# Performance work log

Measured on AMD Instinct MI355X. Metric: run time of the kernel, lower is better.

## Reference

```python
import jax, jax.numpy as jnp
import numpy as np
import math

D_MODEL = 512

def setup_inputs() -> dict:
    key = jax.random.key(0)
    k1, k2, k3 = jax.random.split(key, 3)
    X = jax.random.normal(k1, (4, 8192, D_MODEL), dtype=jnp.float32)
    # nn.Linear(d, d, bias=False) weights, applied as x @ W.T
    s = 1.0 / math.sqrt(D_MODEL)
    W_v = jax.random.uniform(k2, (D_MODEL, D_MODEL), dtype=jnp.float32, minval=-s, maxval=s)
    W_theta = jax.random.uniform(k3, (D_MODEL, D_MODEL), dtype=jnp.float32, minval=-s, maxval=s)
    return {"X": X, "W_v": W_v, "W_theta": W_theta}

def reference(X, W_v, W_theta):
    # X: [B, n, d]
    n = X.shape[1]
    d = X.shape[2]
    XW_v = X @ W_v.T            # [B, n, d]
    theta_X = X @ W_theta.T     # [B, n, d]
    # first term: (1/n) * ones(n,n) @ XW_v == column mean broadcast over rows
    first_term = jnp.mean(XW_v, axis=1, keepdims=True)  # [B, 1, d], broadcasts
    # second term: (1/(n*sqrt(d))) * (X @ theta_X^T) @ XW_v
    # associativity-reduced: theta_X^T @ XW_v is [B, d, d]
    kv = jnp.einsum('bnd,bne->bde', theta_X, XW_v)       # [B, d, d]
    second_term = (X @ kv) / (n * math.sqrt(d))          # [B, n, d]
    return first_term + second_term
```

## Files before the change

kernel.cpp:

```cpp
#include <hip/hip_runtime.h>
#include <stdint.h>


typedef __bf16 bf16x8 __attribute__((ext_vector_type(8)));
typedef float f32x4 __attribute__((ext_vector_type(4)));
typedef unsigned short u16x4 __attribute__((ext_vector_type(4)));
typedef unsigned short u16x8 __attribute__((ext_vector_type(8)));

#define BM 128
#define BN 128
#define BK 32

__device__ __forceinline__ unsigned short f2bf(float f) {
  union { float f; unsigned int u; } c; c.f = f;
  unsigned int u = c.u;
  return (unsigned short)((u + 0x7FFFu + ((u >> 16) & 1u)) >> 16);
}
__device__ __forceinline__ float bf2f(unsigned short h) {
  union { unsigned int u; float f; } c; c.u = ((unsigned int)h) << 16;
  return c.f;
}

__device__ __forceinline__ void gld16(const void* g, void* l) {
  using gptr_t = const __attribute__((address_space(1))) void*;
  using lptr_t = __attribute__((address_space(3))) void*;
  __builtin_amdgcn_global_load_lds((gptr_t)(uintptr_t)g,
                                   (lptr_t)(uint32_t)(uintptr_t)l, 16, 0, 0);
}

__device__ __forceinline__ void gemm_tile(const unsigned short* __restrict__ A, int lda,
                                          const unsigned short* __restrict__ B, int ldb,
                                          int K, int m0, int n0, f32x4 (&acc)[4][4],
                                          bool sameAB) {
  __shared__ unsigned short sA[2][BM * BK];
  __shared__ unsigned short sB[2][BN * BK];
  const int tid = threadIdx.x;
  const int lane = tid & 63;
  const int w = tid >> 6;
  const int wm = w >> 1, wn = w & 1;
  const int quad = lane >> 4, l16 = lane & 15;

#pragma unroll
  for (int mi = 0; mi < 4; mi++)
#pragma unroll
    for (int ni = 0; ni < 4; ni++) acc[mi][ni] = f32x4{0.f, 0.f, 0.f, 0.f};

  for (int kt = 0; kt < K; kt += 2 * BK) {
#pragma unroll
    for (int h = 0; h < 2; h++) {
#pragma unroll
      for (int j = 0; j < 2; j++) {
        const int slot = w * 128 + j * 64 + lane;
        const int row = slot >> 2;
        const int col = (slot & 3) * 8;
        const int kc = kt + h * BK + col;
        gld16(A + (size_t)(m0 + row) * lda + kc,
              (char*)sA[h] + (size_t)(w * 128 + j * 64) * 16);
        if (!sameAB)
          gld16(B + (size_t)(n0 + row) * ldb + kc,
                (char*)sB[h] + (size_t)(w * 128 + j * 64) * 16);
      }
    }
    __syncthreads();

#pragma unroll
    for (int h = 0; h < 2; h++) {
      const unsigned short* bs = sameAB ? sA[h] : sB[h];
      bf16x8 af[4], bfr[4];
#pragma unroll
      for (int mi = 0; mi < 4; mi++)
        af[mi] = *(const bf16x8*)&sA[h][(wm * 64 + mi * 16 + l16) * BK + quad * 8];
#pragma unroll
      for (int ni = 0; ni < 4; ni++)
        bfr[ni] = *(const bf16x8*)&bs[(wn * 64 + ni * 16 + l16) * BK + quad * 8];
#pragma unroll
      for (int mi = 0; mi < 4; mi++)
#pragma unroll
        for (int ni = 0; ni < 4; ni++)
          acc[mi][ni] = __builtin_amdgcn_mfma_f32_16x16x32_bf16(af[mi], bfr[ni],
                                                                acc[mi][ni], 0, 0, 0);
    }
    __syncthreads();
  }
}

__global__ __launch_bounds__(256) void prep_kernel(const float* __restrict__ X,
                                                   unsigned short* __restrict__ Xb,
                                                   unsigned short* __restrict__ Xt) {
  __shared__ unsigned short sT[64 * 64];
  const int t = threadIdx.x;
  const int n0 = blockIdx.x * 64, d0 = blockIdx.y * 64;
  const int b = n0 >> 13, nb = n0 & 8191;
  const int r0 = (t >> 4) * 4, c0 = (t & 15) * 4;
  f32x4 v[4];
#pragma unroll
  for (int i = 0; i < 4; i++)
    v[i] = *(const f32x4*)(X + (size_t)(n0 + r0 + i) * 512 + d0 + c0);
#pragma unroll
  for (int i = 0; i < 4; i++) {
    u16x4 o;
#pragma unroll
    for (int j = 0; j < 4; j++) o[j] = f2bf(v[i][j]);
    *(u16x4*)(Xb + (size_t)(n0 + r0 + i) * 512 + d0 + c0) = o;
  }
#pragma unroll
  for (int j = 0; j < 4; j++) {
    u16x4 wv;
#pragma unroll
    for (int i = 0; i < 4; i++) wv[i] = f2bf(v[i][j]);
    const int c = c0 + j;
    const int rsw = r0 ^ (c & 0x38);
    *(u16x4*)&sT[c * 64 + rsw] = wv;
  }
  __syncthreads();
  const int cr = t >> 3, p = t & 7;
#pragma unroll
  for (int h = 0; h < 2; h++) {
    const int c = cr + h * 32;
    const int phys = (p * 8) ^ (c & 0x38);
    u16x8 val = *(const u16x8*)&sT[c * 64 + phys];
    *(u16x8*)(Xt + (size_t)(b * 512 + d0 + c) * 8192 + nb + p * 8) = val;
  }
}

__global__ __launch_bounds__(256) void prep_w_kernel(const float* __restrict__ Wv,
                                                     const float* __restrict__ Wth,
                                                     unsigned short* __restrict__ Wvb,
                                                     unsigned short* __restrict__ Wtb) {
  const int blk = blockIdx.x;
  const int t = threadIdx.x;
  const float* src = (blk < 128) ? Wv : Wth;
  unsigned short* dst = (blk < 128) ? Wvb : Wtb;
  const int i = (blk & 127) * 256 + t;
  const f32x4* pp = (const f32x4*)(src + (size_t)i * 8);
  f32x4 v0 = pp[0], v1 = pp[1];
  u16x8 o;
  o[0] = f2bf(v0[0]); o[1] = f2bf(v0[1]); o[2] = f2bf(v0[2]); o[3] = f2bf(v0[3]);
  o[4] = f2bf(v1[0]); o[5] = f2bf(v1[1]); o[6] = f2bf(v1[2]); o[7] = f2bf(v1[3]);
  *(u16x8*)(dst + (size_t)i * 8) = o;
}

static __device__ const int TI[10] = {0, 0, 0, 0, 1, 1, 1, 2, 2, 3};
static __device__ const int TJ[10] = {0, 1, 2, 3, 1, 2, 3, 2, 3, 3};

__global__ __launch_bounds__(256) void g_gemm_kernel(const unsigned short* __restrict__ Xt,
                                                     float* __restrict__ G_part) {
  const int t = blockIdx.x;
  const int z = blockIdx.y;
  const int b = z >> 4, s = z & 15;
  const int m0 = TI[t] * 128, n0 = TJ[t] * 128;
  const unsigned short* A = Xt + (size_t)b * 512 * 8192 + (size_t)s * 512;
  f32x4 acc[4][4];
  gemm_tile(A, 8192, A, 8192, 512, m0, n0, acc, m0 == n0);
  float* Cp = G_part + ((size_t)z * 10 + t) * 16384;
  const int tid = threadIdx.x, lane = tid & 63, w = tid >> 6;
  const int wm = w >> 1, wn = w & 1, quad = lane >> 4, l16 = lane & 15;
#pragma unroll
  for (int mi = 0; mi < 4; mi++)
#pragma unroll
    for (int ni = 0; ni < 4; ni++) {
      const int ml = wm * 64 + mi * 16 + quad * 4;
      const int nl = wn * 64 + ni * 16 + l16;
      *(f32x4*)(Cp + (size_t)nl * 128 + ml) = acc[mi][ni];
    }
}

__global__ __launch_bounds__(256) void g_fin_kernel(const float* __restrict__ G_part,
                                                    unsigned short* __restrict__ Gb) {
  const int blk = blockIdx.x;
  const int b = blk / 80, rem = blk % 80;
  const int t = rem >> 3, cc = rem & 7;
  const int i = TI[t], j = TJ[t];
  const int m0 = i * 128, n0 = j * 128;
  const int tid = threadIdx.x;
  const int np = cc * 16 + (tid >> 4);
  const int mp = (tid & 15) * 8;
  f32x4 s0 = f32x4{0.f, 0.f, 0.f, 0.f}, s1 = f32x4{0.f, 0.f, 0.f, 0.f};
#pragma unroll
  for (int s = 0; s < 16; s++) {
    const float* p = G_part + (((size_t)(b * 16 + s)) * 10 + t) * 16384 + (size_t)np * 128 + mp;
    s0 += *(const f32x4*)p;
    s1 += *(const f32x4*)(p + 4);
  }
  const float scale = (float)(1.0 / (8192.0 * 22.627416997969522));
  unsigned short h[8];
#pragma unroll
  for (int r = 0; r < 4; r++) { h[r] = f2bf(s0[r] * scale); h[r + 4] = f2bf(s1[r] * scale); }
  unsigned short* Gbb = Gb + (size_t)b * 262144;
#pragma unroll
  for (int r = 0; r < 8; r++)
    Gbb[(size_t)(m0 + mp + r) * 512 + (n0 + np)] = h[r];
  if (i != j) {
    u16x8 o;
#pragma unroll
    for (int r = 0; r < 8; r++) o[r] = h[r];
    *(u16x8*)(Gbb + (size_t)(n0 + np) * 512 + (m0 + mp)) = o;
  }
}

__global__ __launch_bounds__(256) void gemm_rm_kernel(const unsigned short* __restrict__ A,
                                                      const unsigned short* __restrict__ B,
                                                      unsigned short* __restrict__ C,
                                                      size_t Abs, size_t Bbs) {
  const int b = blockIdx.z;
  const int m0 = blockIdx.x * BM, n0 = blockIdx.y * BN;
  f32x4 acc[4][4];
  gemm_tile(A + (size_t)b * Abs, 512, B + (size_t)b * Bbs, 512, 512, m0, n0, acc, false);
  unsigned short* Cb = C + (size_t)b * 262144;
  const int tid = threadIdx.x, lane = tid & 63, w = tid >> 6;
  const int wm = w >> 1, wn = w & 1, quad = lane >> 4, l16 = lane & 15;
#pragma unroll
  for (int mi = 0; mi < 4; mi++)
#pragma unroll
    for (int ni = 0; ni < 4; ni++) {
      const int m = m0 + wm * 64 + mi * 16 + quad * 4;
      const int n = n0 + wn * 64 + ni * 16 + l16;
#pragma unroll
      for (int r = 0; r < 4; r++)
        Cb[(size_t)(m + r) * 512 + n] = f2bf(acc[mi][ni][r]);
    }
}

__global__ __launch_bounds__(256) void gemm_out_kernel(
    const unsigned short* __restrict__ Xb, const unsigned short* __restrict__ kvt,
    const float* __restrict__ meanV, float* __restrict__ out) {
  const int m0 = blockIdx.x * BM, n0 = blockIdx.y * BN;
  const int b = blockIdx.x >> 6;
  const unsigned short* Bm = kvt + (size_t)b * 262144;
  f32x4 acc[4][4];
  gemm_tile(Xb, 512, Bm, 512, 512, m0, n0, acc, false);
  const int tid = threadIdx.x, lane = tid & 63, w = tid >> 6;
  const int wm = w >> 1, wn = w & 1, quad = lane >> 4, l16 = lane & 15;
#pragma unroll
  for (int ni = 0; ni < 4; ni++) {
    const int e = n0 + wn * 64 + ni * 16 + l16;
    const float mu = meanV[b * 512 + e];
#pragma unroll
    for (int mi = 0; mi < 4; mi++) {
      const int m = m0 + wm * 64 + mi * 16 + quad * 4;
#pragma unroll
      for (int r = 0; r < 4; r++)
        out[(size_t)(m + r) * 512 + e] = acc[mi][ni][r] + mu;
    }
  }
}

__global__ __launch_bounds__(256) void meanx_kernel(const unsigned short* __restrict__ Xt,
                                                    float* __restrict__ mean_x) {
  const int be = blockIdx.x;
  const unsigned short* row = Xt + (size_t)be * 8192;
  const int t = threadIdx.x;
  float s = 0.f;
  for (int c = t; c < 1024; c += 256) {
    u16x8 v = *(const u16x8*)(row + c * 8);
#pragma unroll
    for (int j = 0; j < 8; j++) s += bf2f(v[j]);
  }
  __shared__ float red[256];
  red[t] = s;
  __syncthreads();
  for (int st = 128; st > 0; st >>= 1) {
    if (t < st) red[t] += red[t + st];
    __syncthreads();
  }
  if (t == 0) mean_x[be] = red[0] * (1.f / 8192.f);
}

__global__ __launch_bounds__(256) void meanv_kernel(const float* __restrict__ mean_x,
                                                    const float* __restrict__ Wv,
                                                    float* __restrict__ meanV) {
  const int idx = blockIdx.x * 256 + threadIdx.x;
  const int b = idx >> 9, e = idx & 511;
  const float* mx = mean_x + b * 512;
  const float* wr = Wv + (size_t)e * 512;
  float s = 0.f;
  for (int d = 0; d < 512; d += 4) {
    f32x4 a = *(const f32x4*)(mx + d);
    f32x4 w = *(const f32x4*)(wr + d);
    s += a[0] * w[0] + a[1] * w[1] + a[2] * w[2] + a[3] * w[3];
  }
  meanV[idx] = s;
}

extern "C" void kernel_launch(void* const* d_in, const int* in_sizes, int n_in,
                              void* d_out, int out_size, void* d_ws, size_t ws_size,
                              hipStream_t stream) {
  const float* X = (const float*)d_in[0];
  const float* Wv = (const float*)d_in[1];
  const float* Wth = (const float*)d_in[2];
  float* out = (float*)d_out;
  char* ws = (char*)d_ws;

  unsigned short* Xb = (unsigned short*)(ws);
  unsigned short* Xt = (unsigned short*)(ws + 33554432ull);
  float* G_part = (float*)(ws + 67108864ull);
  unsigned short* Gb = (unsigned short*)(ws + 109051904ull);
  unsigned short* Ht = (unsigned short*)(ws + 111149056ull);
  unsigned short* kvt = (unsigned short*)(ws + 113246208ull);
  unsigned short* Wvb = (unsigned short*)(ws + 115343360ull);
  unsigned short* Wtb = (unsigned short*)(ws + 115867648ull);
  float* mean_x = (float*)(ws + 116391936ull);
  float* meanV = (float*)(ws + 116400128ull);

  prep_w_kernel<<<256, 256, 0, stream>>>(Wv, Wth, Wvb, Wtb);
  prep_kernel<<<dim3(512, 8), 256, 0, stream>>>(X, Xb, Xt);

  g_gemm_kernel<<<dim3(10, 64), 256, 0, stream>>>(Xt, G_part);
  meanx_kernel<<<2048, 256, 0, stream>>>(Xt, mean_x);
  meanv_kernel<<<8, 256, 0, stream>>>(mean_x, Wv, meanV);
  g_fin_kernel<<<320, 256, 0, stream>>>(G_part, Gb);

  gemm_rm_kernel<<<dim3(4, 4, 4), 256, 0, stream>>>(Wvb, Gb, Ht, 0, 262144);
  gemm_rm_kernel<<<dim3(4, 4, 4), 256, 0, stream>>>(Ht, Wtb, kvt, 262144, 0);

  gemm_out_kernel<<<dim3(256, 4), 256, 0, stream>>>(Xb, kvt, meanV, out);
}
```

Before: 252.5 us.

## Software-pipeline GEMM LDS staging and fuse mean computation into prep and finalize

The shared GEMM tile loop now issues the next K-half's global-to-LDS loads before computing the current half, using explicit vmcnt waits and barriers in place of full syncthreads, so memory latency overlaps with MFMA work. The column-mean of X is accumulated with atomics inside prep_kernel, which now handles 128 rows per block, and the separate meanx kernel that re-read Xt is removed. The meanV matvec is folded into extra blocks of g_fin_kernel. Together these cut two launches and one full pass over Xt. In exchange, the mean becomes an atomic float sum whose order is nondeterministic, and the hand-written waitcnt counts must match the number of loads actually issued.

```diff
diff --git a/kernel.cpp b/kernel.cpp
--- a/kernel.cpp
+++ b/kernel.cpp
@@ -10,6 +10,11 @@
 #define BM 128
 #define BN 128
 #define BK 32
+
+#define VM4 asm volatile("s_waitcnt vmcnt(4)" ::: "memory")
+#define VM2 asm volatile("s_waitcnt vmcnt(2)" ::: "memory")
+#define VM0 asm volatile("s_waitcnt vmcnt(0)" ::: "memory")
+#define BAR asm volatile("s_barrier" ::: "memory")
 
 __device__ __forceinline__ unsigned short f2bf(float f) {
   union { float f; unsigned int u; } c; c.f = f;
@@ -45,90 +50,129 @@
 #pragma unroll
     for (int ni = 0; ni < 4; ni++) acc[mi][ni] = f32x4{0.f, 0.f, 0.f, 0.f};
 
+  auto stage = [&](int bb, int kk) {
+#pragma unroll
+    for (int j = 0; j < 2; j++) {
+      const int slot = w * 128 + j * 64 + lane;
+      const int row = slot >> 2;
+      const int col = (slot & 3) * 8;
+      gld16(A + (size_t)(m0 + row) * lda + kk + col,
+            (char*)sA[bb] + (size_t)(w * 128 + j * 64) * 16);
+      if (!sameAB)
+        gld16(B + (size_t)(n0 + row) * ldb + kk + col,
+              (char*)sB[bb] + (size_t)(w * 128 + j * 64) * 16);
+    }
+  };
+
+  auto compute = [&](int bb) {
+    const unsigned short* as = sA[bb];
+    const unsigned short* bs = sameAB ? sA[bb] : sB[bb];
+    bf16x8 af[4], bfr[4];
+#pragma unroll
+    for (int mi = 0; mi < 4; mi++)
+      af[mi] = *(const bf16x8*)&as[(wm * 64 + mi * 16 + l16) * BK + quad * 8];
+#pragma unroll
+    for (int ni = 0; ni < 4; ni++)
+      bfr[ni] = *(const bf16x8*)&bs[(wn * 64 + ni * 16 + l16) * BK + quad * 8];
+#pragma unroll
+    for (int mi = 0; mi < 4; mi++)
+#pragma unroll
+      for (int ni = 0; ni < 4; ni++)
+        acc[mi][ni] = __builtin_amdgcn_mfma_f32_16x16x32_bf16(af[mi], bfr[ni],
+                                                              acc[mi][ni], 0, 0, 0);
+  };
+
+  stage(0, 0);
   for (int kt = 0; kt < K; kt += 2 * BK) {
-#pragma unroll
-    for (int h = 0; h < 2; h++) {
-#pragma unroll
-      for (int j = 0; j < 2; j++) {
-        const int slot = w * 128 + j * 64 + lane;
-        const int row = slot >> 2;
-        const int col = (slot & 3) * 8;
-        const int kc = kt + h * BK + col;
-        gld16(A + (size_t)(m0 + row) * lda + kc,
-              (char*)sA[h] + (size_t)(w * 128 + j * 64) * 16);
-        if (!sameAB)
-          gld16(B + (size_t)(n0 + row) * ldb + kc,
-                (char*)sB[h] + (size_t)(w * 128 + j * 64) * 16);
-      }
-    }
-    __syncthreads();
-
-#pragma unroll
-    for (int h = 0; h < 2; h++) {
-      const unsigned short* bs = sameAB ? sA[h] : sB[h];
-      bf16x8 af[4], bfr[4];
-#pragma unroll
-      for (int mi = 0; mi < 4; mi++)
-        af[mi] = *(const bf16x8*)&sA[h][(wm * 64 + mi * 16 + l16) * BK + quad * 8];
-#pragma unroll
-      for (int ni = 0; ni < 4; ni++)
-        bfr[ni] = *(const bf16x8*)&bs[(wn * 64 + ni * 16 + l16) * BK + quad * 8];
-#pragma unroll
-      for (int mi = 0; mi < 4; mi++)
-#pragma unroll
-        for (int ni = 0; ni < 4; ni++)
-          acc[mi][ni] = __builtin_amdgcn_mfma_f32_16x16x32_bf16(af[mi], bfr[ni],
-                                                                acc[mi][ni], 0, 0, 0);
-    }
-    __syncthreads();
+    stage(1, kt + BK);
+    if (sameAB) { VM2; } else { VM4; }
+    BAR;
+    compute(0);
+    BAR;
+    if (kt + 2 * BK < K) {
+      stage(0, kt + 2 * BK);
+      if (sameAB) { VM2; } else { VM4; }
+    } else {
+      VM0;
+    }
+    BAR;
+    compute(1);
+    BAR;
   }
 }
 
 __global__ __launch_bounds__(256) void prep_kernel(const float* __restrict__ X,
                                                    unsigned short* __restrict__ Xb,
-                                                   unsigned short* __restrict__ Xt) {
-  __shared__ unsigned short sT[64 * 64];
+                                                   unsigned short* __restrict__ Xt,
+                                                   float* __restrict__ mean_x) {
+  __shared__ unsigned short sT[2][64 * 64];
   const int t = threadIdx.x;
-  const int n0 = blockIdx.x * 64, d0 = blockIdx.y * 64;
+  const int n0 = blockIdx.x * 128, d0 = blockIdx.y * 64;
   const int b = n0 >> 13, nb = n0 & 8191;
   const int r0 = (t >> 4) * 4, c0 = (t & 15) * 4;
-  f32x4 v[4];
-#pragma unroll
-  for (int i = 0; i < 4; i++)
-    v[i] = *(const f32x4*)(X + (size_t)(n0 + r0 + i) * 512 + d0 + c0);
-#pragma unroll
-  for (int i = 0; i < 4; i++) {
-    u16x4 o;
-#pragma unroll
-    for (int j = 0; j < 4; j++) o[j] = f2bf(v[i][j]);
-    *(u16x4*)(Xb + (size_t)(n0 + r0 + i) * 512 + d0 + c0) = o;
-  }
-#pragma unroll
-  for (int j = 0; j < 4; j++) {
-    u16x4 wv;
-#pragma unroll
-    for (int i = 0; i < 4; i++) wv[i] = f2bf(v[i][j]);
-    const int c = c0 + j;
-    const int rsw = r0 ^ (c & 0x38);
-    *(u16x4*)&sT[c * 64 + rsw] = wv;
-  }
+  f32x4 v[2][4];
+#pragma unroll
+  for (int s = 0; s < 2; s++)
+#pragma unroll
+    for (int i = 0; i < 4; i++)
+      v[s][i] = *(const f32x4*)(X + (size_t)(n0 + s * 64 + r0 + i) * 512 + d0 + c0);
+#pragma unroll
+  for (int s = 0; s < 2; s++)
+#pragma unroll
+    for (int i = 0; i < 4; i++) {
+      u16x4 o;
+#pragma unroll
+      for (int j = 0; j < 4; j++) o[j] = f2bf(v[s][i][j]);
+      *(u16x4*)(Xb + (size_t)(n0 + s * 64 + r0 + i) * 512 + d0 + c0) = o;
+    }
+#pragma unroll
+  for (int s = 0; s < 2; s++)
+#pragma unroll
+    for (int j = 0; j < 4; j++) {
+      u16x4 wv;
+#pragma unroll
+      for (int i = 0; i < 4; i++) wv[i] = f2bf(v[s][i][j]);
+      const int c = c0 + j;
+      const int rsw = r0 ^ (c & 0x38);
+      *(u16x4*)&sT[s][c * 64 + rsw] = wv;
+    }
   __syncthreads();
   const int cr = t >> 3, p = t & 7;
+  float csum[2] = {0.f, 0.f};
+#pragma unroll
+  for (int s = 0; s < 2; s++)
+#pragma unroll
+    for (int h = 0; h < 2; h++) {
+      const int c = cr + h * 32;
+      const int phys = (p * 8) ^ (c & 0x38);
+      u16x8 val = *(const u16x8*)&sT[s][c * 64 + phys];
+      *(u16x8*)(Xt + (size_t)(b * 512 + d0 + c) * 8192 + nb + s * 64 + p * 8) = val;
+      float ss = 0.f;
+#pragma unroll
+      for (int j = 0; j < 8; j++) ss += bf2f(val[j]);
+      csum[h] += ss;
+    }
 #pragma unroll
   for (int h = 0; h < 2; h++) {
-    const int c = cr + h * 32;
-    const int phys = (p * 8) ^ (c & 0x38);
-    u16x8 val = *(const u16x8*)&sT[c * 64 + phys];
-    *(u16x8*)(Xt + (size_t)(b * 512 + d0 + c) * 8192 + nb + p * 8) = val;
+    float sv = csum[h];
+    sv += __shfl_xor(sv, 1);
+    sv += __shfl_xor(sv, 2);
+    sv += __shfl_xor(sv, 4);
+    if (p == 0) atomicAdd(&mean_x[b * 512 + d0 + cr + h * 32], sv);
   }
 }
 
 __global__ __launch_bounds__(256) void prep_w_kernel(const float* __restrict__ Wv,
                                                      const float* __restrict__ Wth,
                                                      unsigned short* __restrict__ Wvb,
-                                                     unsigned short* __restrict__ Wtb) {
+                                                     unsigned short* __restrict__ Wtb,
+                                                     float* __restrict__ mean_x) {
   const int blk = blockIdx.x;
   const int t = threadIdx.x;
+  if (blk == 0) {
+#pragma unroll
+    for (int i = 0; i < 8; i++) mean_x[t + i * 256] = 0.f;
+  }
   const float* src = (blk < 128) ? Wv : Wth;
   unsigned short* dst = (blk < 128) ? Wvb : Wtb;
   const int i = (blk & 127) * 256 + t;
@@ -166,8 +210,25 @@
 }
 
 __global__ __launch_bounds__(256) void g_fin_kernel(const float* __restrict__ G_part,
-                                                    unsigned short* __restrict__ Gb) {
+                                                    unsigned short* __restrict__ Gb,
+                                                    const float* __restrict__ mean_x,
+                                                    const float* __restrict__ Wv,
+                                                    float* __restrict__ meanV) {
   const int blk = blockIdx.x;
+  if (blk >= 320) {
+    const int idx = (blk - 320) * 256 + threadIdx.x;
+    const int b = idx >> 9, e = idx & 511;
+    const float* mx = mean_x + b * 512;
+    const float* wr = Wv + (size_t)e * 512;
+    float s = 0.f;
+    for (int d = 0; d < 512; d += 4) {
+      f32x4 a = *(const f32x4*)(mx + d);
+      f32x4 w4 = *(const f32x4*)(wr + d);
+      s += a[0] * w4[0] + a[1] * w4[1] + a[2] * w4[2] + a[3] * w4[3];
+    }
+    meanV[idx] = s * (1.f / 8192.f);
+    return;
+  }
   const int b = blk / 80, rem = blk % 80;
   const int t = rem >> 3, cc = rem & 7;
   const int i = TI[t], j = TJ[t];
@@ -245,43 +306,6 @@
   }
 }
 
-__global__ __launch_bounds__(256) void meanx_kernel(const unsigned short* __restrict__ Xt,
-                                                    float* __restrict__ mean_x) {
-  const int be = blockIdx.x;
-  const unsigned short* row = Xt + (size_t)be * 8192;
-  const int t = threadIdx.x;
-  float s = 0.f;
-  for (int c = t; c < 1024; c += 256) {
-    u16x8 v = *(const u16x8*)(row + c * 8);
-#pragma unroll
-    for (int j = 0; j < 8; j++) s += bf2f(v[j]);
-  }
-  __shared__ float red[256];
-  red[t] = s;
-  __syncthreads();
-  for (int st = 128; st > 0; st >>= 1) {
-    if (t < st) red[t] += red[t + st];
-    __syncthreads();
-  }
-  if (t == 0) mean_x[be] = red[0] * (1.f / 8192.f);
-}
-
-__global__ __launch_bounds__(256) void meanv_kernel(const float* __restrict__ mean_x,
-                                                    const float* __restrict__ Wv,
-                                                    float* __restrict__ meanV) {
-  const int idx = blockIdx.x * 256 + threadIdx.x;
-  const int b = idx >> 9, e = idx & 511;
-  const float* mx = mean_x + b * 512;
-  const float* wr = Wv + (size_t)e * 512;
-  float s = 0.f;
-  for (int d = 0; d < 512; d += 4) {
-    f32x4 a = *(const f32x4*)(mx + d);
-    f32x4 w = *(const f32x4*)(wr + d);
-    s += a[0] * w[0] + a[1] * w[1] + a[2] * w[2] + a[3] * w[3];
-  }
-  meanV[idx] = s;
-}
-
 extern "C" void kernel_launch(void* const* d_in, const int* in_sizes, int n_in,
                               void* d_out, int out_size, void* d_ws, size_t ws_size,
                               hipStream_t stream) {
@@ -302,13 +326,11 @@
   float* mean_x = (float*)(ws + 116391936ull);
   float* meanV = (float*)(ws + 116400128ull);
 
-  prep_w_kernel<<<256, 256, 0, stream>>>(Wv, Wth, Wvb, Wtb);
-  prep_kernel<<<dim3(512, 8), 256, 0, stream>>>(X, Xb, Xt);
+  prep_w_kernel<<<256, 256, 0, stream>>>(Wv, Wth, Wvb, Wtb, mean_x);
+  prep_kernel<<<dim3(256, 8), 256, 0, stream>>>(X, Xb, Xt, mean_x);
 
   g_gemm_kernel<<<dim3(10, 64), 256, 0, stream>>>(Xt, G_part);
-  meanx_kernel<<<2048, 256, 0, stream>>>(Xt, mean_x);
-  meanv_kernel<<<8, 256, 0, stream>>>(mean_x, Wv, meanV);
-  g_fin_kernel<<<320, 256, 0, stream>>>(G_part, Gb);
+  g_fin_kernel<<<328, 256, 0, stream>>>(G_part, Gb, mean_x, Wv, meanV);
 
   gemm_rm_kernel<<<dim3(4, 4, 4), 256, 0, stream>>>(Wvb, Gb, Ht, 0, 262144);
   gemm_rm_kernel<<<dim3(4, 4, 4), 256, 0, stream>>>(Ht, Wtb, kvt, 262144, 0);
```

Measured after the change: 241.0 us. -4.6%, faster.
